# Kernel tuning notes

Measured on AMD Instinct MI355X. Metric: run time of the kernel, lower is better.

The kernel has to match this reference:

```python
import jax, jax.numpy as jnp
import numpy as np

WS = 7        # window size
IMG = 56      # input resolution (H = W)
BATCH = 32    # image batch
DIM = 384
HEADS = 12
HEAD_DIM = DIM // HEADS
N = WS * WS                      # tokens per window = 49
NW = (IMG // WS) * (IMG // WS)   # windows per image = 64
B_ = BATCH * NW                  # 2048
TBL = (2 * WS - 1) ** 2          # 169


def _rel_index(ws):
    # standard Swin relative position index, values in [0, (2ws-1)^2)
    coords = np.stack(np.meshgrid(np.arange(ws), np.arange(ws), indexing='ij'))
    coords = coords.reshape(2, -1)                       # (2, N)
    rel = coords[:, :, None] - coords[:, None, :]        # (2, N, N)
    rel = rel.transpose(1, 2, 0).astype(np.int64).copy()
    rel[:, :, 0] += ws - 1
    rel[:, :, 1] += ws - 1
    rel[:, :, 0] *= 2 * ws - 1
    return rel.sum(-1)                                   # (N, N)


def _shift_mask(H, W, ws, shift):
    # shifted-window attention mask, (nW, N, N) with 0 / -100
    img = np.zeros((H, W))
    cnt = 0
    for hs in (slice(0, -ws), slice(-ws, -shift), slice(-shift, None)):
        for wsl in (slice(0, -ws), slice(-ws, -shift), slice(-shift, None)):
            img[hs, wsl] = cnt
            cnt += 1
    win = img.reshape(H // ws, ws, W // ws, ws).transpose(0, 2, 1, 3).reshape(-1, ws * ws)
    diff = win[:, None, :] - win[:, :, None]
    return np.where(diff != 0, -100.0, 0.0).astype(np.float32)


def setup_inputs() -> dict:
    key = jax.random.key(0)
    ks = jax.random.split(key, 7)
    s = 0.02
    return {
        'x': jax.random.normal(ks[0], (B_, N, DIM), jnp.float32),
        'mask': jnp.asarray(_shift_mask(IMG, IMG, WS, WS // 2)),
        'rpe_indices': jnp.asarray(_rel_index(WS)),
        'qkv_w': jax.random.normal(ks[1], (3 * DIM, DIM), jnp.float32) * s,
        'qkv_b': jnp.zeros((3 * DIM,), jnp.float32),
        'proj_w': jax.random.normal(ks[2], (DIM, DIM), jnp.float32) * s,
        'proj_b': jnp.zeros((DIM,), jnp.float32),
        'q_rpe': jax.random.normal(ks[3], (HEADS, HEAD_DIM, TBL), jnp.float32) * s,
        'k_rpe': jax.random.normal(ks[4], (HEADS, HEAD_DIM, TBL), jnp.float32) * s,
        'v_rpe': jax.random.normal(ks[5], (HEADS, TBL, HEAD_DIM), jnp.float32) * s,
    }


def reference(x, mask, rpe_indices, qkv_w, qkv_b, proj_w, proj_b, q_rpe, k_rpe, v_rpe):
    B, n, C = x.shape
    h, hd = q_rpe.shape[0], q_rpe.shape[1]
    scale = hd ** -0.5

    qkv = x @ qkv_w.T + qkv_b                                   # (B, N, 3C)
    qkv = qkv.reshape(B, n, 3, h, hd).transpose(2, 0, 3, 1, 4)   # (3, B, h, N, hd)
    q, k, v = qkv[0] * scale, qkv[1], qkv[2]

    attn = jnp.einsum('bhid,bhjd->bhij', q, k)                   # (B, h, N, N)

    # Contextual q/k bias. The torch code does b_q.flatten(2)[:, :, rpe_indices]
    # with rpe_indices in [0, TBL): gathering from the flattened (N*TBL) axis with
    # indices < TBL selects row 0 of the N axis, i.e. b_q[:, :, 0, rpe_indices].
    # We compute only that row, which is mathematically identical.
    bq0 = jnp.einsum('bhd,hdt->bht', q[:, :, 0], q_rpe)          # (B, h, TBL)
    bk0 = jnp.einsum('bhd,hdt->bht', k[:, :, 0], k_rpe)          # (B, h, TBL)
    attn = attn + (bq0 + bk0)[:, :, rpe_indices]                 # gather -> (B, h, N, N)

    nW = mask.shape[0]
    attn = attn.reshape(B // nW, nW, h, n, n) + mask[None, :, None]
    attn = jax.nn.softmax(attn.reshape(B, h, n, n), axis=-1)

    # contextual v bias: w = v_rpe[:, rpe_indices] -> (h, N, N, hd)
    w = v_rpe[:, rpe_indices.reshape(-1)].reshape(h, n, n, hd)
    r_v = jnp.einsum('bhij,hijd->bihd', attn, w).reshape(B, n, C)

    out = jnp.einsum('bhij,bhjd->bihd', attn, v).reshape(B, n, C) + r_v
    out = out @ proj_w.T + proj_b
    return out, attn
```

## Files before the change

kernel.cpp:

```cpp
#include <hip/hip_runtime.h>


typedef unsigned int u32;
typedef unsigned short u16;
typedef __attribute__((ext_vector_type(8))) short bf16x8;
typedef __attribute__((ext_vector_type(4))) float f32x4;
typedef float f4a __attribute__((ext_vector_type(4), aligned(4)));

#define SCALE 0.17677669529663687f

__device__ __forceinline__ u16 f2b(float f) {
  union { float f; u32 u; } c; c.f = f;
  u32 u = c.u;
  return (u16)((u + 0x7FFFu + ((u >> 16) & 1u)) >> 16);
}
__device__ __forceinline__ float b2f(u16 s) {
  union { float f; u32 u; } c; c.u = ((u32)s) << 16;
  return c.f;
}
__device__ __forceinline__ void async16(void* lds, const void* g) {
  __builtin_amdgcn_global_load_lds(
      (const __attribute__((address_space(1))) u32*)g,
      (__attribute__((address_space(3))) u32*)lds, 16, 0, 0);
}

__global__ __launch_bounds__(256) void k_cast(const float* __restrict__ s,
                                              u16* __restrict__ d, int n4) {
  int i = blockIdx.x * 256 + threadIdx.x;
  int str = gridDim.x * 256;
  for (; i < n4; i += str) {
    float4 v = ((const float4*)s)[i];
    ushort4 o;
    o.x = f2b(v.x); o.y = f2b(v.y); o.z = f2b(v.z); o.w = f2b(v.w);
    ((ushort4*)d)[i] = o;
  }
}

__global__ __launch_bounds__(256) void k_mbi(const float* __restrict__ mask,
                                             const int* __restrict__ idx,
                                             u16* __restrict__ mbi) {
  int i = blockIdx.x * 256 + threadIdx.x;
  if (i >= 64 * 2401) return;
  int p = i % 2401;
  mbi[i] = (u16)(idx[p] | ((mask[i] != 0.0f) ? 256 : 0));
}

__global__ __launch_bounds__(256) void k_qkv(
    const u16* __restrict__ A, const u16* __restrict__ Bw,
    const float* __restrict__ bias, u16* __restrict__ outq) {
  int bx = blockIdx.x;
  int mt = bx / 9, nt = bx - mt * 9;
  size_t m0 = (size_t)mt * 128;
  int n0 = nt * 128;
  int tid = threadIdx.x;
  int w = tid >> 6, l = tid & 63;
  int wm = w >> 1, wn = w & 1;
  int lr = l & 15, lg = l >> 4, lk8 = lg << 3;
  __shared__ u16 At[128 * 32];
  __shared__ u16 Bt[128 * 32];
  f32x4 acc[4][4] = {};
  int row = tid >> 2, c8 = (tid & 3) << 3;
  const u16* gA = A + (m0 + row) * 384 + c8;
  const u16* gA2 = A + (m0 + row + 64) * 384 + c8;
  const u16* gB = Bw + (size_t)(n0 + row) * 384 + c8;
  const u16* gB2 = Bw + (size_t)(n0 + row + 64) * 384 + c8;
  for (int ks = 0; ks < 12; ++ks) {
    int k0 = ks * 32;
    async16(At + tid * 8, gA + k0);
    async16(At + (256 + tid) * 8, gA2 + k0);
    async16(Bt + tid * 8, gB + k0);
    async16(Bt + (256 + tid) * 8, gB2 + k0);
    __syncthreads();
    bf16x8 af[4], bfr[4];
#pragma unroll
    for (int mi = 0; mi < 4; ++mi)
      af[mi] = *(const bf16x8*)&At[(wm * 64 + mi * 16 + lr) * 32 + lk8];
#pragma unroll
    for (int ni = 0; ni < 4; ++ni)
      bfr[ni] = *(const bf16x8*)&Bt[(wn * 64 + ni * 16 + lr) * 32 + lk8];
#pragma unroll
    for (int mi = 0; mi < 4; ++mi)
#pragma unroll
      for (int ni = 0; ni < 4; ++ni)
        acc[mi][ni] = __builtin_amdgcn_mfma_f32_16x16x32_bf16(af[mi], bfr[ni], acc[mi][ni], 0, 0, 0);
    __syncthreads();
  }
#pragma unroll
  for (int ni = 0; ni < 4; ++ni) {
    int cc = n0 + wn * 64 + ni * 16 + lr;
    float bv = bias[cc];
    float sc = (cc < 384) ? SCALE : 1.0f;
#pragma unroll
    for (int mi = 0; mi < 4; ++mi)
#pragma unroll
      for (int r = 0; r < 4; ++r) {
        size_t rr = m0 + wm * 64 + mi * 16 + lg * 4 + r;
        outq[rr * 1152 + cc] = f2b((acc[mi][ni][r] + bv) * sc);
      }
  }
}

__global__ __launch_bounds__(256) void k_attn(
    const u16* __restrict__ qkv,
    const float* __restrict__ q_rpe, const float* __restrict__ k_rpe,
    const u16* __restrict__ mbi,
    float* __restrict__ attn, u16* __restrict__ o1) {
  int blk = blockIdx.x;
  int b = blk / 3, hg = blk % 3;
  int tid = threadIdx.x, w = tid >> 6, l = tid & 63;
  int h = hg * 4 + w;
  int lr = l & 15, g = l >> 4;

  __shared__ u16 mbiL[2408];
  __shared__ __align__(16) u16 vL[4][2048];
  __shared__ __align__(16) u16 pL[4][4096];
  __shared__ float bqkL[4][172];

  const u16* qbase = qkv + (size_t)b * 49 * 1152 + h * 32;
  const u16* kbase = qbase + 384;
  const u16* vbase = qbase + 768;

  {
    const u16* mrow = mbi + (size_t)(b & 63) * 2401;
    for (int p = tid; p < 2401; p += 256) mbiL[p] = mrow[p];
  }
  u16* vw = &vL[w][0];
#pragma unroll
  for (int p = 0; p < 4; ++p) {
    int j = p * 16 + (l >> 2);
    int jr = (j < 49) ? j : 48;
    async16(vw + p * 512 + l * 8, vbase + (size_t)jr * 1152 + (l & 3) * 8);
  }

  bf16x8 qf[4], kf[4];
#pragma unroll
  for (int t = 0; t < 4; ++t) {
    int qi = t * 16 + lr;
    int qir = (qi < 49) ? qi : 48;
    qf[t] = *(const bf16x8*)(qbase + (size_t)qir * 1152 + g * 8);
    kf[t] = *(const bf16x8*)(kbase + (size_t)qir * 1152 + g * 8);
  }

  f32x4 S[4][4] = {};
#pragma unroll
  for (int mt = 0; mt < 4; ++mt)
#pragma unroll
    for (int nt = 0; nt < 4; ++nt)
      S[mt][nt] = __builtin_amdgcn_mfma_f32_16x16x32_bf16(kf[mt], qf[nt], S[mt][nt], 0, 0, 0);

  {
    float q0d[32], k0d[32];
#pragma unroll
    for (int d = 0; d < 32; ++d) { q0d[d] = b2f(qbase[d]); k0d[d] = b2f(kbase[d]); }
#pragma unroll
    for (int t0 = 0; t0 < 192; t0 += 64) {
      int t = t0 + l;
      if (t < 169) {
        float s = 0.f;
#pragma unroll
        for (int d = 0; d < 32; ++d)
          s += q0d[d] * q_rpe[(h * 32 + d) * 169 + t] +
               k0d[d] * k_rpe[(h * 32 + d) * 169 + t];
        bqkL[w][t] = s;
      }
    }
  }
  __syncthreads();

#pragma unroll
  for (int nt = 0; nt < 4; ++nt) {
    int qi = nt * 16 + lr;
#pragma unroll
    for (int mt = 0; mt < 4; ++mt)
#pragma unroll
      for (int r = 0; r < 4; ++r) {
        int kj = mt * 16 + g * 4 + r;
        float s = S[mt][nt][r];
        if (qi < 49 && kj < 49) {
          u16 t = mbiL[qi * 49 + kj];
          s += bqkL[w][t & 255] - 100.f * (float)(t >> 8);
        } else {
          s = -1e9f;
        }
        S[mt][nt][r] = s;
      }
  }

  float rinv[4];
#pragma unroll
  for (int nt = 0; nt < 4; ++nt) {
    float m = -1e30f;
#pragma unroll
    for (int mt = 0; mt < 4; ++mt)
#pragma unroll
      for (int r = 0; r < 4; ++r) m = fmaxf(m, S[mt][nt][r]);
    m = fmaxf(m, __shfl_xor(m, 16, 64));
    m = fmaxf(m, __shfl_xor(m, 32, 64));
    float sum = 0.f;
#pragma unroll
    for (int mt = 0; mt < 4; ++mt)
#pragma unroll
      for (int r = 0; r < 4; ++r) {
        float e = __expf(S[mt][nt][r] - m);
        S[mt][nt][r] = e;
        sum += e;
      }
    sum += __shfl_xor(sum, 16, 64);
    sum += __shfl_xor(sum, 32, 64);
    rinv[nt] = 1.f / sum;
  }

  {
    float* ao = attn + (size_t)(b * 12 + h) * 2401;
#pragma unroll
    for (int nt = 0; nt < 4; ++nt) {
      int qi = nt * 16 + lr;
      if (qi < 49) {
        float riv = rinv[nt];
#pragma unroll
        for (int mt = 0; mt < 3; ++mt) {
          f4a vst;
          vst[0] = S[mt][nt][0] * riv;
          vst[1] = S[mt][nt][1] * riv;
          vst[2] = S[mt][nt][2] * riv;
          vst[3] = S[mt][nt][3] * riv;
          *(f4a*)(ao + qi * 49 + mt * 16 + g * 4) = vst;
        }
        if (g == 0) ao[qi * 49 + 48] = S[3][nt][0] * riv;
      }
    }
  }

  u16* pw = &pL[w][0];
#pragma unroll
  for (int nt = 0; nt < 4; ++nt) {
    int qi = nt * 16 + lr;
    int swz = (qi & 7) << 4;
#pragma unroll
    for (int mt = 0; mt < 4; ++mt) {
      u32 w0 = (u32)f2b(S[mt][nt][0]) | ((u32)f2b(S[mt][nt][1]) << 16);
      u32 w1 = (u32)f2b(S[mt][nt][2]) | ((u32)f2b(S[mt][nt][3]) << 16);
      int off = (qi * 128 + mt * 32 + g * 8) ^ swz;
      uint2 pk = {w0, w1};
      *(uint2*)((char*)pw + off) = pk;
    }
  }

  f32x4 O[2][4] = {};
#pragma unroll
  for (int ks = 0; ks < 2; ++ks) {
    bf16x8 pb[4];
#pragma unroll
    for (int nti = 0; nti < 4; ++nti) {
      int qi = nti * 16 + lr;
      int off = (qi * 128 + ks * 64 + g * 16) ^ ((qi & 7) << 4);
      pb[nti] = *(const bf16x8*)((const char*)pw + off);
    }
    bf16x8 va[2];
#pragma unroll
    for (int mtd = 0; mtd < 2; ++mtd)
#pragma unroll
      for (int jj = 0; jj < 8; ++jj)
        va[mtd][jj] = (short)vw[(ks * 32 + g * 8 + jj) * 32 + mtd * 16 + lr];
#pragma unroll
    for (int mtd = 0; mtd < 2; ++mtd)
#pragma unroll
      for (int nti = 0; nti < 4; ++nti)
        O[mtd][nti] = __builtin_amdgcn_mfma_f32_16x16x32_bf16(va[mtd], pb[nti], O[mtd][nti], 0, 0, 0);
  }

  {
    u16* ob = o1 + (size_t)b * 49 * 384 + h * 32;
#pragma unroll
    for (int nti = 0; nti < 4; ++nti) {
      int i = nti * 16 + lr;
      if (i < 49) {
        float riv = rinv[nti];
#pragma unroll
        for (int mtd = 0; mtd < 2; ++mtd) {
          u32 w0 = (u32)f2b(O[mtd][nti][0] * riv) | ((u32)f2b(O[mtd][nti][1] * riv) << 16);
          u32 w1 = (u32)f2b(O[mtd][nti][2] * riv) | ((u32)f2b(O[mtd][nti][3] * riv) << 16);
          uint2 pk = {w0, w1};
          *(uint2*)&ob[(size_t)i * 384 + mtd * 16 + g * 4] = pk;
        }
      }
    }
  }
}

__global__ __launch_bounds__(256) void k_rv(
    const float* __restrict__ attn, const int* __restrict__ idx,
    const float* __restrict__ v_rpe, u16* __restrict__ o1) {
  int bx = blockIdx.x;
  int bc = bx & 7;
  int hi = bx >> 3;
  int i = hi % 49, h = hi / 49;
  int b0 = bc * 256;
  int tid = threadIdx.x;
  int w = tid >> 6, l = tid & 63;
  int lr = l & 15, g = l >> 4;

  __shared__ __align__(16) u16 aB[256 * 64];
  __shared__ __align__(16) u16 wT[32 * 64];

  if (tid < 196) {
    int j = tid >> 2, d0 = (tid & 3) * 8;
    const float* vr = v_rpe + ((size_t)h * 169 + idx[i * 49 + j]) * 32 + d0;
    float4 a = *(const float4*)vr;
    float4 bvv = *(const float4*)(vr + 4);
    float el[8] = {a.x, a.y, a.z, a.w, bvv.x, bvv.y, bvv.z, bvv.w};
#pragma unroll
    for (int e = 0; e < 8; ++e) {
      int d = d0 + e;
      int byte = (d * 128 + j * 2) ^ ((d & 7) << 4);
      *(u16*)((char*)wT + byte) = f2b(el[e]);
    }
  } else {
    int t = tid - 196;
    int j = 49 + (t >> 2), d0 = (t & 3) * 8;
#pragma unroll
    for (int e = 0; e < 8; ++e) {
      int d = d0 + e;
      int byte = (d * 128 + j * 2) ^ ((d & 7) << 4);
      *(u16*)((char*)wT + byte) = 0;
    }
  }

  {
    int bl = tid;
    const float* ar = attn + ((size_t)(b0 + bl) * 12 + h) * 2401 + (size_t)i * 49;
    f4a fv[12];
#pragma unroll
    for (int q = 0; q < 12; ++q) fv[q] = *(const f4a*)(ar + q * 4);
    float tail = ar[48];
    u32 wd[32];
#pragma unroll
    for (int k = 0; k < 24; ++k)
      wd[k] = (u32)f2b(fv[k >> 1][(k & 1) * 2]) |
              ((u32)f2b(fv[k >> 1][(k & 1) * 2 + 1]) << 16);
    wd[24] = (u32)f2b(tail);
#pragma unroll
    for (int k = 25; k < 32; ++k) wd[k] = 0;
#pragma unroll
    for (int q = 0; q < 8; ++q) {
      int byte = (bl * 128 + q * 16) ^ ((bl & 7) << 4);
      *(uint4*)((char*)aB + byte) = *(uint4*)&wd[q * 4];
    }
  }
  __syncthreads();

  f32x4 acc[2][4] = {};
#pragma unroll
  for (int ks = 0; ks < 2; ++ks) {
    bf16x8 af[2], bfr[4];
#pragma unroll
    for (int mt = 0; mt < 2; ++mt) {
      int d = mt * 16 + lr;
      int byte = (d * 128 + ks * 64 + g * 16) ^ ((d & 7) << 4);
      af[mt] = *(const bf16x8*)((const char*)wT + byte);
    }
#pragma unroll
    for (int nt = 0; nt < 4; ++nt) {
      int row = w * 64 + nt * 16 + lr;
      int byte = (row * 128 + ks * 64 + g * 16) ^ ((row & 7) << 4);
      bfr[nt] = *(const bf16x8*)((const char*)aB + byte);
    }
#pragma unroll
    for (int mt = 0; mt < 2; ++mt)
#pragma unroll
      for (int nt = 0; nt < 4; ++nt)
        acc[mt][nt] = __builtin_amdgcn_mfma_f32_16x16x32_bf16(af[mt], bfr[nt], acc[mt][nt], 0, 0, 0);
  }

#pragma unroll
  for (int nt = 0; nt < 4; ++nt) {
    int bl = w * 64 + nt * 16 + lr;
    u16* ob = o1 + ((size_t)(b0 + bl) * 49 + i) * 384 + h * 32;
#pragma unroll
    for (int mt = 0; mt < 2; ++mt) {
      int d = mt * 16 + g * 4;
      uint2 old = *(uint2*)&ob[d];
      uint2 nw;
      nw.x = (u32)f2b(b2f((u16)(old.x & 0xffff)) + acc[mt][nt][0]) |
             ((u32)f2b(b2f((u16)(old.x >> 16)) + acc[mt][nt][1]) << 16);
      nw.y = (u32)f2b(b2f((u16)(old.y & 0xffff)) + acc[mt][nt][2]) |
             ((u32)f2b(b2f((u16)(old.y >> 16)) + acc[mt][nt][3]) << 16);
      *(uint2*)&ob[d] = nw;
    }
  }
}

__global__ __launch_bounds__(256) void k_proj(
    const u16* __restrict__ A, const u16* __restrict__ Bw,
    const float* __restrict__ bias, float* __restrict__ out) {
  int bx = blockIdx.x;
  int mt = bx / 3, nt = bx - mt * 3;
  size_t m0 = (size_t)mt * 128;
  int n0 = nt * 128;
  int tid = threadIdx.x;
  int w = tid >> 6, l = tid & 63;
  int wm = w >> 1, wn = w & 1;
  int lr = l & 15, lg = l >> 4, lk8 = lg << 3;
  __shared__ u16 At[128 * 32];
  __shared__ u16 Bt[128 * 32];
  f32x4 acc[4][4] = {};
  int row = tid >> 2, c8 = (tid & 3) << 3;
  const u16* gA = A + (m0 + row) * 384 + c8;
  const u16* gA2 = A + (m0 + row + 64) * 384 + c8;
  const u16* gB = Bw + (size_t)(n0 + row) * 384 + c8;
  const u16* gB2 = Bw + (size_t)(n0 + row + 64) * 384 + c8;
  for (int ks = 0; ks < 12; ++ks) {
    int k0 = ks * 32;
    async16(At + tid * 8, gA + k0);
    async16(At + (256 + tid) * 8, gA2 + k0);
    async16(Bt + tid * 8, gB + k0);
    async16(Bt + (256 + tid) * 8, gB2 + k0);
    __syncthreads();
    bf16x8 af[4], bfr[4];
#pragma unroll
    for (int mi = 0; mi < 4; ++mi)
      af[mi] = *(const bf16x8*)&At[(wm * 64 + mi * 16 + lr) * 32 + lk8];
#pragma unroll
    for (int ni = 0; ni < 4; ++ni)
      bfr[ni] = *(const bf16x8*)&Bt[(wn * 64 + ni * 16 + lr) * 32 + lk8];
#pragma unroll
    for (int mi = 0; mi < 4; ++mi)
#pragma unroll
      for (int ni = 0; ni < 4; ++ni)
        acc[mi][ni] = __builtin_amdgcn_mfma_f32_16x16x32_bf16(af[mi], bfr[ni], acc[mi][ni], 0, 0, 0);
    __syncthreads();
  }
#pragma unroll
  for (int mi = 0; mi < 4; ++mi)
#pragma unroll
    for (int ni = 0; ni < 4; ++ni)
#pragma unroll
      for (int r = 0; r < 4; ++r) {
        int rr = wm * 64 + mi * 16 + lg * 4 + r;
        int cc = wn * 64 + ni * 16 + lr;
        out[(m0 + rr) * 384 + (size_t)(n0 + cc)] = acc[mi][ni][r] + bias[n0 + cc];
      }
}

extern "C" void kernel_launch(void* const* d_in, const int* in_sizes, int n_in,
                              void* d_out, int out_size, void* d_ws, size_t ws_size,
                              hipStream_t stream) {
  const float* x      = (const float*)d_in[0];
  const float* mask   = (const float*)d_in[1];
  const int*   rpe    = (const int*)d_in[2];
  const float* qkv_w  = (const float*)d_in[3];
  const float* qkv_b  = (const float*)d_in[4];
  const float* proj_w = (const float*)d_in[5];
  const float* proj_b = (const float*)d_in[6];
  const float* q_rpe  = (const float*)d_in[7];
  const float* k_rpe  = (const float*)d_in[8];
  const float* v_rpe  = (const float*)d_in[9];

  float* out  = (float*)d_out;
  float* attn = out + (size_t)100352 * 384;

  char* ws = (char*)d_ws;
  u16* qkvb   = (u16*)ws;
  u16* wqkvb  = (u16*)(ws + 231211008);
  u16* wprojb = (u16*)(ws + 232095744);
  u16* mbi    = (u16*)(ws + 232390656);
  u16* xb     = (u16*)(ws + 232697984);
  u16* o1     = xb;

  k_cast<<<2048, 256, 0, stream>>>(x, xb, 9633792);
  k_cast<<<432, 256, 0, stream>>>(qkv_w, wqkvb, 110592);
  k_cast<<<144, 256, 0, stream>>>(proj_w, wprojb, 36864);
  k_mbi<<<601, 256, 0, stream>>>(mask, rpe, mbi);
  k_qkv<<<7056, 256, 0, stream>>>(xb, wqkvb, qkv_b, qkvb);
  k_attn<<<6144, 256, 0, stream>>>(qkvb, q_rpe, k_rpe, mbi, attn, o1);
  k_rv<<<4704, 256, 0, stream>>>(attn, rpe, v_rpe, o1);
  k_proj<<<2352, 256, 0, stream>>>(o1, wprojb, proj_b, out);
}
```

Baseline: 646.8 us.

## Precompute q/k RPE bias with batched MFMA kernel and stage attn stores through LDS

Adds a k_bqk kernel that computes the contextual q/k bias rows for all windows and heads as a bf16 MFMA GEMM, writing them into a scratch area of the output buffer. k_attn no longer does the per-wave scalar 32x169 dot products with strided fp32 rpe loads; it just loads the precomputed 169 floats. The attention probability write is also restaged through a reused LDS region so the global stores of the 2401-float rows become contiguous and coalesced instead of scattered 4-wide stores. The cost is an extra launch and round trip through global memory, bf16 rounding of the rpe tables, and reliance on the output region being overwritten later by k_proj.

```diff
diff --git a/kernel.cpp b/kernel.cpp
--- a/kernel.cpp
+++ b/kernel.cpp
@@ -100,9 +100,84 @@
   }
 }
 
+__global__ __launch_bounds__(256) void k_bqk(
+    const u16* __restrict__ qkv, const float* __restrict__ q_rpe,
+    const float* __restrict__ k_rpe, float* __restrict__ bqk) {
+  int bx = blockIdx.x;
+  int mtile = bx / 12, h = bx % 12;
+  int b0 = mtile * 64;
+  int tid = threadIdx.x;
+  int w = tid >> 6, l = tid & 63;
+  int lr = l & 15, g = l >> 4;
+
+  __shared__ __align__(16) u16 At[64 * 64];
+  __shared__ __align__(16) u16 Bt[192 * 64];
+
+  {
+    int m = tid >> 2;
+#pragma unroll
+    for (int rnd = 0; rnd < 2; ++rnd) {
+      int c = (tid & 3) + rnd * 4;
+      const u16* src = qkv + (size_t)(b0 + m) * 56448 + h * 32 +
+                       ((c < 4) ? c * 8 : 384 + (c - 4) * 8);
+      bf16x8 v = *(const bf16x8*)src;
+      int byte = (m * 128 + c * 16) ^ ((m & 7) << 4);
+      *(bf16x8*)((char*)At + byte) = v;
+    }
+  }
+  if (tid < 192) {
+    int t = tid;
+#pragma unroll
+    for (int c = 0; c < 8; ++c) {
+      u16 pk[8];
+#pragma unroll
+      for (int e = 0; e < 8; ++e) {
+        int d = (c & 3) * 8 + e;
+        float v = 0.f;
+        if (t < 169)
+          v = (c < 4) ? q_rpe[(h * 32 + d) * 169 + t]
+                      : k_rpe[(h * 32 + d) * 169 + t];
+        pk[e] = f2b(v);
+      }
+      int byte = (t * 128 + c * 16) ^ ((t & 7) << 4);
+      *(bf16x8*)((char*)Bt + byte) = *(bf16x8*)pk;
+    }
+  }
+  __syncthreads();
+
+  f32x4 acc[12] = {};
+  bf16x8 af[2];
+#pragma unroll
+  for (int ks = 0; ks < 2; ++ks) {
+    int row = w * 16 + lr;
+    af[ks] = *(const bf16x8*)((const char*)At +
+              ((row * 128 + ks * 64 + g * 16) ^ ((row & 7) << 4)));
+  }
+#pragma unroll
+  for (int nt = 0; nt < 12; ++nt) {
+#pragma unroll
+    for (int ks = 0; ks < 2; ++ks) {
+      int t = nt * 16 + lr;
+      bf16x8 bf = *(const bf16x8*)((const char*)Bt +
+                   ((t * 128 + ks * 64 + g * 16) ^ ((t & 7) << 4)));
+      acc[nt] = __builtin_amdgcn_mfma_f32_16x16x32_bf16(af[ks], bf, acc[nt], 0, 0, 0);
+    }
+  }
+#pragma unroll
+  for (int nt = 0; nt < 12; ++nt) {
+    int t = nt * 16 + lr;
+    if (t < 169) {
+#pragma unroll
+      for (int r = 0; r < 4; ++r) {
+        int b = b0 + w * 16 + g * 4 + r;
+        bqk[((size_t)b * 12 + h) * 169 + t] = acc[nt][r];
+      }
+    }
+  }
+}
+
 __global__ __launch_bounds__(256) void k_attn(
-    const u16* __restrict__ qkv,
-    const float* __restrict__ q_rpe, const float* __restrict__ k_rpe,
+    const u16* __restrict__ qkv, const float* __restrict__ bqkG,
     const u16* __restrict__ mbi,
     float* __restrict__ attn, u16* __restrict__ o1) {
   int blk = blockIdx.x;
@@ -111,10 +186,12 @@
   int h = hg * 4 + w;
   int lr = l & 15, g = l >> 4;
 
-  __shared__ u16 mbiL[2408];
+  __shared__ __align__(16) char R[32704];
   __shared__ __align__(16) u16 vL[4][2048];
-  __shared__ __align__(16) u16 pL[4][4096];
-  __shared__ float bqkL[4][172];
+  u16* mbiL = (u16*)R;
+  float* bqkL = (float*)(R + 4832);
+  u16* pL = (u16*)(R + 7600);
+  float* aS = (float*)R;
 
   const u16* qbase = qkv + (size_t)b * 49 * 1152 + h * 32;
   const u16* kbase = qbase + 384;
@@ -130,6 +207,14 @@
     int j = p * 16 + (l >> 2);
     int jr = (j < 49) ? j : 48;
     async16(vw + p * 512 + l * 8, vbase + (size_t)jr * 1152 + (l & 3) * 8);
+  }
+  {
+    const float* bg = bqkG + ((size_t)b * 12 + h) * 169;
+#pragma unroll
+    for (int t0 = 0; t0 < 192; t0 += 64) {
+      int t = t0 + l;
+      if (t < 169) bqkL[w * 172 + t] = bg[t];
+    }
   }
 
   bf16x8 qf[4], kf[4];
@@ -148,23 +233,6 @@
     for (int nt = 0; nt < 4; ++nt)
       S[mt][nt] = __builtin_amdgcn_mfma_f32_16x16x32_bf16(kf[mt], qf[nt], S[mt][nt], 0, 0, 0);
 
-  {
-    float q0d[32], k0d[32];
-#pragma unroll
-    for (int d = 0; d < 32; ++d) { q0d[d] = b2f(qbase[d]); k0d[d] = b2f(kbase[d]); }
-#pragma unroll
-    for (int t0 = 0; t0 < 192; t0 += 64) {
-      int t = t0 + l;
-      if (t < 169) {
-        float s = 0.f;
-#pragma unroll
-        for (int d = 0; d < 32; ++d)
-          s += q0d[d] * q_rpe[(h * 32 + d) * 169 + t] +
-               k0d[d] * k_rpe[(h * 32 + d) * 169 + t];
-        bqkL[w][t] = s;
-      }
-    }
-  }
   __syncthreads();
 
 #pragma unroll
@@ -178,7 +246,7 @@
         float s = S[mt][nt][r];
         if (qi < 49 && kj < 49) {
           u16 t = mbiL[qi * 49 + kj];
-          s += bqkL[w][t & 255] - 100.f * (float)(t >> 8);
+          s += bqkL[w * 172 + (t & 255)] - 100.f * (float)(t >> 8);
         } else {
           s = -1e9f;
         }
@@ -210,39 +278,20 @@
     rinv[nt] = 1.f / sum;
   }
 
-  {
-    float* ao = attn + (size_t)(b * 12 + h) * 2401;
-#pragma unroll
-    for (int nt = 0; nt < 4; ++nt) {
-      int qi = nt * 16 + lr;
-      if (qi < 49) {
-        float riv = rinv[nt];
-#pragma unroll
-        for (int mt = 0; mt < 3; ++mt) {
-          f4a vst;
-          vst[0] = S[mt][nt][0] * riv;
-          vst[1] = S[mt][nt][1] * riv;
-          vst[2] = S[mt][nt][2] * riv;
-          vst[3] = S[mt][nt][3] * riv;
-          *(f4a*)(ao + qi * 49 + mt * 16 + g * 4) = vst;
-        }
-        if (g == 0) ao[qi * 49 + 48] = S[3][nt][0] * riv;
-      }
-    }
-  }
-
-  u16* pw = &pL[w][0];
+  u16* pw = pL + w * 3136;
 #pragma unroll
   for (int nt = 0; nt < 4; ++nt) {
     int qi = nt * 16 + lr;
-    int swz = (qi & 7) << 4;
-#pragma unroll
-    for (int mt = 0; mt < 4; ++mt) {
-      u32 w0 = (u32)f2b(S[mt][nt][0]) | ((u32)f2b(S[mt][nt][1]) << 16);
-      u32 w1 = (u32)f2b(S[mt][nt][2]) | ((u32)f2b(S[mt][nt][3]) << 16);
-      int off = (qi * 128 + mt * 32 + g * 8) ^ swz;
-      uint2 pk = {w0, w1};
-      *(uint2*)((char*)pw + off) = pk;
+    if (qi < 49) {
+      int swz = (qi & 7) << 4;
+#pragma unroll
+      for (int mt = 0; mt < 4; ++mt) {
+        u32 w0 = (u32)f2b(S[mt][nt][0]) | ((u32)f2b(S[mt][nt][1]) << 16);
+        u32 w1 = (u32)f2b(S[mt][nt][2]) | ((u32)f2b(S[mt][nt][3]) << 16);
+        int off = (qi * 128 + mt * 32 + g * 8) ^ swz;
+        uint2 pk = {w0, w1};
+        *(uint2*)((char*)pw + off) = pk;
+      }
     }
   }
 
@@ -253,7 +302,8 @@
 #pragma unroll
     for (int nti = 0; nti < 4; ++nti) {
       int qi = nti * 16 + lr;
-      int off = (qi * 128 + ks * 64 + g * 16) ^ ((qi & 7) << 4);
+      int qir = (qi < 49) ? qi : 48;
+      int off = (qir * 128 + ks * 64 + g * 16) ^ ((qir & 7) << 4);
       pb[nti] = *(const bf16x8*)((const char*)pw + off);
     }
     bf16x8 va[2];
@@ -285,6 +335,39 @@
         }
       }
     }
+  }
+
+  __syncthreads();
+  float* aw = aS + w * 1216;
+  float* ao = attn + (size_t)(b * 12 + h) * 2401;
+#pragma unroll
+  for (int half = 0; half < 2; ++half) {
+    int lo = half * 1204;
+#pragma unroll
+    for (int nt = 0; nt < 4; ++nt) {
+      int qi = nt * 16 + lr;
+      if (qi < 49) {
+        float riv = rinv[nt];
+#pragma unroll
+        for (int mt = 0; mt < 4; ++mt)
+#pragma unroll
+          for (int r = 0; r < 4; ++r) {
+            int kj = mt * 16 + g * 4 + r;
+            if (kj < 49) {
+              int p = qi * 49 + kj - lo;
+              if (p >= 0 && p < 1204) aw[p] = S[mt][nt][r] * riv;
+            }
+          }
+      }
+    }
+    asm volatile("s_waitcnt lgkmcnt(0)" ::: "memory");
+    int lim = half ? 1197 : 1204;
+#pragma unroll
+    for (int it = 0; it < 19; ++it) {
+      int p = l + it * 64;
+      if (p < lim) ao[lo + p] = aw[p];
+    }
+    asm volatile("s_waitcnt lgkmcnt(0)" ::: "memory");
   }
 }
 
@@ -458,6 +541,7 @@
 
   float* out  = (float*)d_out;
   float* attn = out + (size_t)100352 * 384;
+  float* bqkG = out;
 
   char* ws = (char*)d_ws;
   u16* qkvb   = (u16*)ws;
@@ -472,7 +556,8 @@
   k_cast<<<144, 256, 0, stream>>>(proj_w, wprojb, 36864);
   k_mbi<<<601, 256, 0, stream>>>(mask, rpe, mbi);
   k_qkv<<<7056, 256, 0, stream>>>(xb, wqkvb, qkv_b, qkvb);
-  k_attn<<<6144, 256, 0, stream>>>(qkvb, q_rpe, k_rpe, mbi, attn, o1);
+  k_bqk<<<384, 256, 0, stream>>>(qkvb, q_rpe, k_rpe, bqkG);
+  k_attn<<<6144, 256, 0, stream>>>(qkvb, bqkG, mbi, attn, o1);
   k_rv<<<4704, 256, 0, stream>>>(attn, rpe, v_rpe, o1);
   k_proj<<<2352, 256, 0, stream>>>(o1, wprojb, proj_b, out);
 }
```

Result: faster. 589.2 us (-8.9%).
